# Kernel optimization log

Measured on AMD Instinct MI355X. Metric: run time of the kernel, lower is better.

## Reference

```python
import jax, jax.numpy as jnp
import numpy as np

N = 100000      # nodes
E = 3200000     # edges
F_IN = 128      # input node features
G = 64          # graphs in batch
A = 32          # action_shape


def _fanin_uniform(key, shape):
    v = 1.0 / np.sqrt(shape[0])
    return jax.random.uniform(key, shape, jnp.float32, -v, v)


def setup_inputs() -> dict:
    key = jax.random.key(0)
    ks = jax.random.split(key, 16)
    x = jax.random.normal(ks[0], (N, F_IN), jnp.float32)
    edge_index = jax.random.randint(ks[1], (2, E), 0, N, jnp.int64)
    batch = jnp.sort(jax.random.randint(ks[2], (N,), 0, G, jnp.int64))
    init_w = 0.003
    return {
        "x": x,
        "edge_index": edge_index,
        "batch": batch,
        # GCN weights are [in, out] (old-style PyG GCNConv .weight)
        "W1": _fanin_uniform(ks[3], (F_IN, 16)), "b1": jnp.zeros((16,), jnp.float32),
        "W2": _fanin_uniform(ks[4], (16, 64)),   "b2": jnp.zeros((64,), jnp.float32),
        "W3": _fanin_uniform(ks[5], (64, 32)),   "b3": jnp.zeros((32,), jnp.float32),
        # MLP head (Linear stores [out, in]; we keep [in, out] and matmul directly)
        "Wa": _fanin_uniform(ks[6], (32, 64)),   "ba": jnp.zeros((64,), jnp.float32),
        "Wo": jax.random.uniform(ks[7], (64, A), jnp.float32, -init_w, init_w),
        "bo": jnp.zeros((A,), jnp.float32),
    }


def _gcn_conv(x, W, b, src, dst, dinv):
    # GCNConv: D^{-1/2}(A+I)D^{-1/2} X W + b, symmetric norm with self-loops.
    h = x @ W                                   # [N, out] small GEMM
    coef = dinv[src] * dinv[dst]                # [E]
    msg = h[src] * coef[:, None]                # gather + scale (memory-bound)
    agg = jax.ops.segment_sum(msg, dst, num_segments=N)  # scatter-add
    agg = agg + h * (dinv * dinv)[:, None]      # self-loop contribution
    return agg + b


def reference(x, edge_index, batch, W1, b1, W2, b2, W3, b3, Wa, ba, Wo, bo):
    src, dst = edge_index[0], edge_index[1]
    # degree with self-loops (edge weights = 1)
    deg = jax.ops.segment_sum(jnp.ones((E,), x.dtype), dst, num_segments=N) + 1.0
    dinv = jax.lax.rsqrt(deg)

    h = jax.nn.relu(_gcn_conv(x, W1, b1, src, dst, dinv))   # dropout: eval no-op
    h = jax.nn.relu(_gcn_conv(h, W2, b2, src, dst, dinv))
    h = _gcn_conv(h, W3, b3, src, dst, dinv)                # [N, 32]

    # global_mean_pool over batch ids
    sums = jax.ops.segment_sum(h, batch, num_segments=G)            # [G, 32]
    cnts = jax.ops.segment_sum(jnp.ones((N,), h.dtype), batch, num_segments=G)
    pooled = sums / jnp.maximum(cnts, 1.0)[:, None]

    a = jax.nn.relu(pooled @ Wa + ba)
    return jnp.tanh(a @ Wo + bo)                             # [G, A]
```

## Files before the change

### kernel.cpp

```cpp
#include <hip/hip_runtime.h>
#include <hip/hip_bf16.h>
#include <math.h>


#define THREADS 256
#define TCSR 1024
#define BSH 8
#define MAXNB 512
#define CH_E 4096
#define CPT 8

typedef __attribute__((ext_vector_type(8))) short short8;
typedef __attribute__((ext_vector_type(4))) float f32x4;

__device__ inline unsigned short f2bf(float f) {
    unsigned int u = __float_as_uint(f);
    return (unsigned short)((u + 0x7fffu + ((u >> 16) & 1u)) >> 16);
}
__device__ inline unsigned int pk2bf(float a, float b) {
    return (unsigned int)f2bf(a) | ((unsigned int)f2bf(b) << 16);
}
__device__ inline float bflo(unsigned int u) { return __uint_as_float(u << 16); }
__device__ inline float bfhi(unsigned int u) { return __uint_as_float(u & 0xffff0000u); }
__device__ inline void unpk8(const uint4 u, float* f) {
    f[0] = bflo(u.x); f[1] = bfhi(u.x); f[2] = bflo(u.y); f[3] = bfhi(u.y);
    f[4] = bflo(u.z); f[5] = bfhi(u.z); f[6] = bflo(u.w); f[7] = bfhi(u.w);
}

__global__ void k_countA(const int* __restrict__ dst, unsigned short* __restrict__ lp16,
                         int* __restrict__ cnt_mat, int E, int NB, int NCH) {
    __shared__ int hist[MAXNB];
    int t = threadIdx.x, chunk = blockIdx.x;
    for (int h = t; h < NB; h += THREADS) hist[h] = 0;
    __syncthreads();
    int e0 = chunk * CH_E, e1 = min(E, e0 + CH_E);
    for (int e = e0 + t; e < e1; e += THREADS) {
        int h = dst[e] >> BSH;
        int lp = atomicAdd(&hist[h], 1);
        lp16[e] = (unsigned short)lp;
    }
    __syncthreads();
    for (int h = t; h < NB; h += THREADS) cnt_mat[(size_t)h * NCH + chunk] = hist[h];
}

__global__ void k_sumK1(const int* __restrict__ cnt_mat, int* __restrict__ bucket_tot, int NCH) {
    __shared__ int red[THREADS];
    int b = blockIdx.x, t = threadIdx.x;
    int s = 0;
    for (int c = t; c < NCH; c += THREADS) s += cnt_mat[(size_t)b * NCH + c];
    red[t] = s;
    __syncthreads();
    for (int off = THREADS / 2; off > 0; off >>= 1) {
        if (t < off) red[t] += red[t + off];
        __syncthreads();
    }
    if (t == 0) bucket_tot[b] = red[0];
}

__global__ void k_scanK2(const int* __restrict__ bucket_tot, int* __restrict__ bucket_base,
                         int* __restrict__ rowptr, float* __restrict__ sums,
                         int NB, int E, int N, int GS) {
    __shared__ int sh[MAXNB];
    int t = threadIdx.x;
    for (int i = t; i < GS; i += MAXNB) sums[i] = 0.0f;
    int v = (t < NB) ? bucket_tot[t] : 0;
    sh[t] = v;
    __syncthreads();
    for (int off = 1; off < MAXNB; off <<= 1) {
        int u = (t >= off) ? sh[t - off] : 0;
        __syncthreads();
        sh[t] += u;
        __syncthreads();
    }
    if (t < NB) bucket_base[t] = sh[t] - v;
    if (t == 0) { bucket_base[NB] = E; rowptr[N] = E; }
}

__global__ void k_scanK3(const int* __restrict__ cnt_mat, const int* __restrict__ bucket_base,
                         int* __restrict__ offs_mat, int NCH) {
    __shared__ int sh[THREADS];
    int b = blockIdx.x, t = threadIdx.x;
    int c0 = t * CPT;
    int v[CPT];
    int s = 0;
#pragma unroll
    for (int k = 0; k < CPT; ++k) {
        int c = c0 + k;
        v[k] = (c < NCH) ? cnt_mat[(size_t)b * NCH + c] : 0;
        s += v[k];
    }
    sh[t] = s;
    __syncthreads();
    for (int off = 1; off < THREADS; off <<= 1) {
        int u = (t >= off) ? sh[t - off] : 0;
        __syncthreads();
        sh[t] += u;
        __syncthreads();
    }
    int run = bucket_base[b] + sh[t] - s;
#pragma unroll
    for (int k = 0; k < CPT; ++k) {
        int c = c0 + k;
        if (c < NCH) { offs_mat[(size_t)b * NCH + c] = run; run += v[k]; }
    }
}

__global__ void k_scatter2(const int* __restrict__ src, const int* __restrict__ dst,
                           const unsigned short* __restrict__ lp16,
                           const int* __restrict__ offs_mat,
                           unsigned int* __restrict__ bedges, int E, int NB, int NCH) {
    __shared__ int offs[MAXNB];
    int t = threadIdx.x, chunk = blockIdx.x;
    for (int h = t; h < NB; h += THREADS) offs[h] = offs_mat[(size_t)h * NCH + chunk];
    __syncthreads();
    int e0 = chunk * CH_E, e1 = min(E, e0 + CH_E);
    for (int e = e0 + t; e < e1; e += THREADS) {
        int d = dst[e];
        int h = d >> BSH;
        int pos = offs[h] + (int)lp16[e];
        bedges[pos] = ((unsigned int)src[e] << BSH) | (unsigned int)(d & ((1 << BSH) - 1));
    }
}

__global__ __launch_bounds__(1024) void k_bucket_csr(const unsigned int* __restrict__ bedges,
                             const int* __restrict__ bucket_base,
                             int* __restrict__ rowptr, float* __restrict__ dinv,
                             int* __restrict__ csr_src, int N) {
    __shared__ int hist[256];
    __shared__ int sc[256];
    __shared__ int cur[256];
    int t = threadIdx.x;
    int b = blockIdx.x;
    int base = bucket_base[b];
    int end = bucket_base[b + 1];
    if (t < 256) hist[t] = 0;
    __syncthreads();
    for (int i = base + t; i < end; i += TCSR)
        atomicAdd(&hist[bedges[i] & 255], 1);
    __syncthreads();
    int c = 0;
    if (t < 256) { c = hist[t]; sc[t] = c; }
    __syncthreads();
    for (int off = 1; off < 256; off <<= 1) {
        int u = (t >= off && t < 256) ? sc[t - off] : 0;
        __syncthreads();
        if (t < 256) sc[t] += u;
        __syncthreads();
    }
    if (t < 256) {
        int excl = sc[t] - c;
        int node = (b << BSH) + t;
        if (node < N) {
            rowptr[node] = base + excl;
            dinv[node] = (float)(1.0 / sqrt((double)(c + 1)));
        }
        cur[t] = excl;
    }
    __syncthreads();
    for (int i = base + t; i < end; i += TCSR) {
        unsigned int u = bedges[i];
        int ln = (int)(u & 255);
        int p = atomicAdd(&cur[ln], 1);
        csr_src[base + p] = (int)(u >> BSH);
    }
}

__global__ __launch_bounds__(256) void k_gemm1(const float* __restrict__ X,
                        const float* __restrict__ W,
                        const float* __restrict__ dinv, unsigned short* __restrict__ H, int N) {
    __shared__ float Wt[16 * 128];
    int t = threadIdx.x;
    for (int i = t; i < 16 * 128; i += THREADS) {
        int j = i >> 7, k = i & 127;
        Wt[i] = W[k * 16 + j];
    }
    __syncthreads();
    int q = t & 3;
    int row = blockIdx.x * 64 + (t >> 2);
    if (row >= N) return;
    const float4* xr = (const float4*)(X + (size_t)row * 128);
    float acc[16];
#pragma unroll
    for (int j = 0; j < 16; ++j) acc[j] = 0.0f;
#pragma unroll
    for (int i = 0; i < 8; ++i) {
        int k4 = q + 4 * i;
        float4 xv = xr[k4];
#pragma unroll
        for (int j = 0; j < 16; ++j) {
            const float4 wv = *(const float4*)&Wt[j * 128 + k4 * 4];
            acc[j] += xv.x * wv.x + xv.y * wv.y + xv.z * wv.z + xv.w * wv.w;
        }
    }
#pragma unroll
    for (int j = 0; j < 16; ++j) {
        acc[j] += __shfl_xor(acc[j], 1);
        acc[j] += __shfl_xor(acc[j], 2);
    }
    if (q == 0) {
        float di = dinv[row];
        uint4 oa, ob;
        oa.x = pk2bf(acc[0] * di, acc[1] * di);
        oa.y = pk2bf(acc[2] * di, acc[3] * di);
        oa.z = pk2bf(acc[4] * di, acc[5] * di);
        oa.w = pk2bf(acc[6] * di, acc[7] * di);
        ob.x = pk2bf(acc[8] * di, acc[9] * di);
        ob.y = pk2bf(acc[10] * di, acc[11] * di);
        ob.z = pk2bf(acc[12] * di, acc[13] * di);
        ob.w = pk2bf(acc[14] * di, acc[15] * di);
        uint4* outr = (uint4*)(H + (size_t)row * 16);
        outr[0] = oa;
        outr[1] = ob;
    }
}

template<int F, int MODE, int S>
__global__ __launch_bounds__(256) void k_pull(
        const int* __restrict__ rowptr, const int* __restrict__ csr_src,
        const float* __restrict__ dinv, const unsigned short* __restrict__ Hb,
        const float* __restrict__ bias, void* __restrict__ outp,
        const int* __restrict__ batch, float* __restrict__ gsums,
        int N, int G) {
    const int LPN = F / 8;
    const int GRP = LPN * S;
    const int NPB = THREADS / GRP;
    int t = threadIdx.x;
    int idx = t % GRP;
    int fl = idx % LPN;
    int s  = idx / LPN;
    int fo = fl * 8;
    int node = blockIdx.x * NPB + t / GRP;

    float acc[8] = {0.f, 0.f, 0.f, 0.f, 0.f, 0.f, 0.f, 0.f};
    if (node < N) {
        int beg = rowptr[node], end = rowptr[node + 1];
        int i = beg + s;
        for (; i + 3 * S < end; i += 4 * S) {
            int s0 = csr_src[i];
            int s1 = csr_src[i + S];
            int s2 = csr_src[i + 2 * S];
            int s3 = csr_src[i + 3 * S];
            uint4 g0 = *(const uint4*)(Hb + (size_t)s0 * F + fo);
            uint4 g1 = *(const uint4*)(Hb + (size_t)s1 * F + fo);
            uint4 g2 = *(const uint4*)(Hb + (size_t)s2 * F + fo);
            uint4 g3 = *(const uint4*)(Hb + (size_t)s3 * F + fo);
            float f0[8], f1[8], f2[8], f3[8];
            unpk8(g0, f0); unpk8(g1, f1); unpk8(g2, f2); unpk8(g3, f3);
#pragma unroll
            for (int j = 0; j < 8; ++j) acc[j] += (f0[j] + f1[j]) + (f2[j] + f3[j]);
        }
        for (; i < end; i += S) {
            int sv = csr_src[i];
            uint4 g = *(const uint4*)(Hb + (size_t)sv * F + fo);
            float f[8];
            unpk8(g, f);
#pragma unroll
            for (int j = 0; j < 8; ++j) acc[j] += f[j];
        }
    }
#pragma unroll
    for (int j = 0; j < 8; ++j) {
        if (S >= 2) acc[j] += __shfl_xor(acc[j], LPN);
        if (S >= 4) acc[j] += __shfl_xor(acc[j], 2 * LPN);
    }

    if constexpr (MODE == 3) {
        __shared__ float lsum[4][32];
        __shared__ int g0s;
        for (int z = t; z < 4 * 32; z += THREADS) ((float*)lsum)[z] = 0.0f;
        if (t == 0) g0s = batch[blockIdx.x * NPB];
        __syncthreads();
        int g0 = g0s;
        if (node < N && s == 0) {
            uint4 gs = *(const uint4*)(Hb + (size_t)node * F + fo);
            float sf[8];
            unpk8(gs, sf);
            float di = dinv[node];
            int g = batch[node];
            int r = g - g0;
            if ((unsigned)r < 4u) {
#pragma unroll
                for (int j = 0; j < 8; ++j)
                    atomicAdd(&lsum[r][fo + j], di * (acc[j] + sf[j]));
            } else {
#pragma unroll
                for (int j = 0; j < 8; ++j)
                    atomicAdd(&gsums[(size_t)g * 32 + fo + j], di * (acc[j] + sf[j]));
            }
        }
        __syncthreads();
        if (t < 128) {
            int r = t >> 5, f = t & 31;
            int g = g0 + r;
            float v = lsum[r][f];
            if (g < G && v != 0.0f) atomicAdd(&gsums[(size_t)g * 32 + f], v);
        }
    } else {
        if (node < N && s == 0) {
            uint4 gs = *(const uint4*)(Hb + (size_t)node * F + fo);
            float sf[8];
            unpk8(gs, sf);
            float di = dinv[node];
            float tv[8];
#pragma unroll
            for (int j = 0; j < 8; ++j) tv[j] = di * (acc[j] + sf[j]);
            if constexpr (MODE == 1) {
                float w[8];
#pragma unroll
                for (int j = 0; j < 8; ++j) w[j] = fmaxf(tv[j] + bias[fo + j], 0.0f) * di;
                uint4 st;
                st.x = pk2bf(w[0], w[1]); st.y = pk2bf(w[2], w[3]);
                st.z = pk2bf(w[4], w[5]); st.w = pk2bf(w[6], w[7]);
                *(uint4*)((unsigned short*)outp + (size_t)node * F + fo) = st;
            } else {
                uint4 st;
                st.x = pk2bf(tv[0], tv[1]); st.y = pk2bf(tv[2], tv[3]);
                st.z = pk2bf(tv[4], tv[5]); st.w = pk2bf(tv[6], tv[7]);
                *(uint4*)((unsigned short*)outp + (size_t)node * F + fo) = st;
            }
        }
    }
}

__global__ __launch_bounds__(256) void k_mlp(const unsigned short* __restrict__ P2b,
                      const float* __restrict__ W2, const float* __restrict__ b2,
                      const float* __restrict__ W3, const float* __restrict__ dinv,
                      unsigned short* __restrict__ Hb3, int N) {
    __shared__ unsigned int aTd[4][32][17];
    int t = threadIdx.x;
    int w = t >> 6;
    int l = t & 63;
    int g = l >> 4;
    int c = l & 15;
    int node = blockIdx.x * 64 + w * 16 + c;
    bool nv = node < N;
    int cn = nv ? node : 0;

    short8 w2f[4];
#pragma unroll
    for (int mi = 0; mi < 4; ++mi) {
        short8 f = {0, 0, 0, 0, 0, 0, 0, 0};
        if (g < 2) {
            int j = 16 * mi + c;
#pragma unroll
            for (int e = 0; e < 8; ++e)
                f[e] = (short)f2bf(W2[(8 * g + e) * 64 + j]);
        }
        w2f[mi] = f;
    }
    short8 w3f[2][2];
#pragma unroll
    for (int mt = 0; mt < 2; ++mt)
#pragma unroll
        for (int kt = 0; kt < 2; ++kt) {
            short8 f;
#pragma unroll
            for (int e = 0; e < 8; ++e)
                f[e] = (short)f2bf(W3[(32 * kt + 8 * g + e) * 32 + 16 * mt + c]);
            w3f[mt][kt] = f;
        }
    float b2v[16];
#pragma unroll
    for (int mi = 0; mi < 4; ++mi)
#pragma unroll
        for (int r = 0; r < 4; ++r)
            b2v[4 * mi + r] = b2[16 * mi + 4 * g + r];

    short8 pf = {0, 0, 0, 0, 0, 0, 0, 0};
    if (g < 2) {
        pf = *(const short8*)(P2b + (size_t)cn * 16 + 8 * g);
    }

    f32x4 zero = {0.f, 0.f, 0.f, 0.f};
    f32x4 acc1[4];
#pragma unroll
    for (int mi = 0; mi < 4; ++mi)
        acc1[mi] = __builtin_amdgcn_mfma_f32_16x16x32_bf16(w2f[mi], pf, zero, 0, 0, 0);

#pragma unroll
    for (int mi = 0; mi < 4; ++mi) {
        float a0 = fmaxf(acc1[mi][0] + b2v[4 * mi + 0], 0.f);
        float a1 = fmaxf(acc1[mi][1] + b2v[4 * mi + 1], 0.f);
        float a2 = fmaxf(acc1[mi][2] + b2v[4 * mi + 2], 0.f);
        float a3 = fmaxf(acc1[mi][3] + b2v[4 * mi + 3], 0.f);
        aTd[w][8 * mi + 2 * g][c]     = pk2bf(a0, a1);
        aTd[w][8 * mi + 2 * g + 1][c] = pk2bf(a2, a3);
    }
    __syncthreads();

    short8 bfr[2];
#pragma unroll
    for (int kt = 0; kt < 2; ++kt) {
        short8 f;
#pragma unroll
        for (int i = 0; i < 4; ++i) {
            unsigned int d = aTd[w][16 * kt + 4 * g + i][c];
            f[2 * i]     = (short)(d & 0xffffu);
            f[2 * i + 1] = (short)(d >> 16);
        }
        bfr[kt] = f;
    }

    f32x4 acc2[2] = {{0.f, 0.f, 0.f, 0.f}, {0.f, 0.f, 0.f, 0.f}};
#pragma unroll
    for (int mt = 0; mt < 2; ++mt)
#pragma unroll
        for (int kt = 0; kt < 2; ++kt)
            acc2[mt] = __builtin_amdgcn_mfma_f32_16x16x32_bf16(w3f[mt][kt], bfr[kt], acc2[mt], 0, 0, 0);

    if (nv) {
        float di = dinv[node];
        unsigned short* o = Hb3 + (size_t)node * 32;
#pragma unroll
        for (int mt = 0; mt < 2; ++mt) {
            *(unsigned int*)(o + 16 * mt + 4 * g)     = pk2bf(acc2[mt][0] * di, acc2[mt][1] * di);
            *(unsigned int*)(o + 16 * mt + 4 * g + 2) = pk2bf(acc2[mt][2] * di, acc2[mt][3] * di);
        }
    }
}

__global__ void k_head(const float* __restrict__ sums, const int* __restrict__ batch, int N,
                       const float* __restrict__ b3,
                       const float* __restrict__ Wa, const float* __restrict__ ba,
                       const float* __restrict__ Wo, const float* __restrict__ bo,
                       float* __restrict__ out) {
    int g = blockIdx.x;
    int j = threadIdx.x;
    int lo = 0, hi = N;
    while (lo < hi) { int m = (lo + hi) >> 1; if (batch[m] < g) lo = m + 1; else hi = m; }
    int start = lo;
    lo = start; hi = N;
    while (lo < hi) { int m = (lo + hi) >> 1; if (batch[m] < g + 1) lo = m + 1; else hi = m; }
    int cnt = lo - start;
    float inv = 1.0f / (float)(cnt > 0 ? cnt : 1);

    __shared__ float p[32];
    __shared__ float a[64];
    if (j < 32) p[j] = sums[g * 32 + j] * inv + b3[j];
    __syncthreads();
    float acc = ba[j];
#pragma unroll
    for (int k = 0; k < 32; ++k) acc += p[k] * Wa[k * 64 + j];
    a[j] = fmaxf(acc, 0.0f);
    __syncthreads();
    if (j < 32) {
        float acc2 = bo[j];
#pragma unroll
        for (int k = 0; k < 64; ++k) acc2 += a[k] * Wo[k * 32 + j];
        out[g * 32 + j] = tanhf(acc2);
    }
}

static inline int cdiv(long long a, int b) { return (int)((a + b - 1) / b); }
static inline size_t align256(size_t x) { return (x + 255) & ~(size_t)255; }

extern "C" void kernel_launch(void* const* d_in, const int* in_sizes, int n_in,
                              void* d_out, int out_size, void* d_ws, size_t ws_size,
                              hipStream_t stream) {
    const float* x     = (const float*)d_in[0];
    const int*   edge  = (const int*)d_in[1];
    const int*   batch = (const int*)d_in[2];
    const float* W1 = (const float*)d_in[3];  const float* b1 = (const float*)d_in[4];
    const float* W2 = (const float*)d_in[5];  const float* b2 = (const float*)d_in[6];
    const float* W3 = (const float*)d_in[7];  const float* b3 = (const float*)d_in[8];
    const float* Wa = (const float*)d_in[9];  const float* ba = (const float*)d_in[10];
    const float* Wo = (const float*)d_in[11]; const float* bo = (const float*)d_in[12];

    const int E = in_sizes[1] / 2;
    const int N = in_sizes[2];
    const int G = 64;
    const int NB = cdiv(N, 1 << BSH);
    const int NCH = cdiv(E, CH_E);

    const int* srcp = edge;
    const int* dstp = edge + E;

    char* base = (char*)d_ws;
    size_t off = 0;
    float* dinv   = (float*)(base + off); off = align256(off + sizeof(float) * N);
    unsigned short* lp16 = (unsigned short*)(base + off); off = align256(off + sizeof(short) * E);
    int* cnt_mat  = (int*)(base + off); off = align256(off + sizeof(int) * (size_t)NB * NCH);
    int* offs_mat = (int*)(base + off); off = align256(off + sizeof(int) * (size_t)NB * NCH);
    int* btot     = (int*)(base + off); off = align256(off + sizeof(int) * (NB + 1));
    int* bbase    = (int*)(base + off); off = align256(off + sizeof(int) * (NB + 1));
    unsigned int* bedges = (unsigned int*)(base + off); off = align256(off + sizeof(int) * E);
    int* rowptr   = (int*)(base + off); off = align256(off + sizeof(int) * (N + 1));
    int* csr_src  = (int*)(base + off); off = align256(off + sizeof(int) * E);
    unsigned short* Hb1 = (unsigned short*)(base + off); off = align256(off + sizeof(short) * (size_t)N * 16);
    unsigned short* Hb2 = (unsigned short*)(base + off); off = align256(off + sizeof(short) * (size_t)N * 16);
    unsigned short* P2b = (unsigned short*)(base + off); off = align256(off + sizeof(short) * (size_t)N * 16);
    unsigned short* Hb3 = (unsigned short*)(base + off); off = align256(off + sizeof(short) * (size_t)N * 32);
    float* sums   = (float*)(base + off); off = align256(off + sizeof(float) * G * 32);

    k_countA<<<NCH, THREADS, 0, stream>>>(dstp, lp16, cnt_mat, E, NB, NCH);
    k_sumK1<<<NB, THREADS, 0, stream>>>(cnt_mat, btot, NCH);
    k_scanK2<<<1, MAXNB, 0, stream>>>(btot, bbase, rowptr, sums, NB, E, N, G * 32);
    k_scanK3<<<NB, THREADS, 0, stream>>>(cnt_mat, bbase, offs_mat, NCH);
    k_scatter2<<<NCH, THREADS, 0, stream>>>(srcp, dstp, lp16, offs_mat, bedges, E, NB, NCH);

    k_bucket_csr<<<NB, TCSR, 0, stream>>>(bedges, bbase, rowptr, dinv, csr_src, N);

    k_gemm1<<<cdiv(N, 64), THREADS, 0, stream>>>(x, W1, dinv, Hb1, N);
    k_pull<16, 1, 4><<<cdiv(N, 32), THREADS, 0, stream>>>(rowptr, csr_src, dinv, Hb1, b1, Hb2,
                                                          nullptr, nullptr, N, G);

    k_pull<16, 2, 4><<<cdiv(N, 32), THREADS, 0, stream>>>(rowptr, csr_src, dinv, Hb2, nullptr, P2b,
                                                          nullptr, nullptr, N, G);

    k_mlp<<<cdiv(N, 64), THREADS, 0, stream>>>(P2b, W2, b2, W3, dinv, Hb3, N);

    k_pull<32, 3, 2><<<cdiv(N, 32), THREADS, 0, stream>>>(rowptr, csr_src, dinv, Hb3, nullptr,
                                                          nullptr, batch, sums, N, G);

    k_head<<<G, 64, 0, stream>>>(sums, batch, N, b3, Wa, ba, Wo, bo, (float*)d_out);
}
```

Measured before the change: 307.5 us.

## Stage bucket scatter and CSR writes in LDS for coalesced global stores

The edge scatter kernel now computes per-chunk bucket offsets with an in-block scan and places the packed edges into shared memory in bucket order. It then writes them to global memory in runs that are contiguous within each bucket, instead of random scattered stores. The bucket CSR kernel likewise builds each bucket's sorted source list in LDS when it fits within a capacity, then copies it out contiguously. This adds more LDS (about 36KB and 35KB), an extra block scan and extra barriers, which may reduce occupancy.

```diff
diff --git a/kernel.cpp b/kernel.cpp
--- a/kernel.cpp
+++ b/kernel.cpp
@@ -9,6 +9,7 @@
 #define MAXNB 512
 #define CH_E 4096
 #define CPT 8
+#define CSR_CAP 8704
 
 typedef __attribute__((ext_vector_type(8))) short short8;
 typedef __attribute__((ext_vector_type(4))) float f32x4;
@@ -105,21 +106,47 @@
     }
 }
 
-__global__ void k_scatter2(const int* __restrict__ src, const int* __restrict__ dst,
-                           const unsigned short* __restrict__ lp16,
-                           const int* __restrict__ offs_mat,
-                           unsigned int* __restrict__ bedges, int E, int NB, int NCH) {
+__global__ __launch_bounds__(256) void k_scatter2(
+        const int* __restrict__ src, const int* __restrict__ dst,
+        const unsigned short* __restrict__ lp16,
+        const int* __restrict__ cnt_mat, const int* __restrict__ offs_mat,
+        unsigned int* __restrict__ bedges, int E, int NB, int NCH) {
     __shared__ int offs[MAXNB];
+    __shared__ int excl[MAXNB];
+    __shared__ unsigned int wbuf[CH_E];
+    __shared__ int gbuf[CH_E];
     int t = threadIdx.x, chunk = blockIdx.x;
-    for (int h = t; h < NB; h += THREADS) offs[h] = offs_mat[(size_t)h * NCH + chunk];
+    int c0 = (t < NB) ? cnt_mat[(size_t)t * NCH + chunk] : 0;
+    int c1 = (t + 256 < NB) ? cnt_mat[(size_t)(t + 256) * NCH + chunk] : 0;
+    if (t < NB) offs[t] = offs_mat[(size_t)t * NCH + chunk];
+    if (t + 256 < NB) offs[t + 256] = offs_mat[(size_t)(t + 256) * NCH + chunk];
+    excl[t] = c0;
+    excl[t + 256] = c1;
+    __syncthreads();
+    for (int off = 1; off < MAXNB; off <<= 1) {
+        int a = (t >= off) ? excl[t - off] : 0;
+        int b = (t + 256 >= off) ? excl[t + 256 - off] : 0;
+        __syncthreads();
+        excl[t] += a;
+        excl[t + 256] += b;
+        __syncthreads();
+    }
+    excl[t] -= c0;
+    excl[t + 256] -= c1;
     __syncthreads();
     int e0 = chunk * CH_E, e1 = min(E, e0 + CH_E);
+    int len = e1 - e0;
     for (int e = e0 + t; e < e1; e += THREADS) {
         int d = dst[e];
         int h = d >> BSH;
-        int pos = offs[h] + (int)lp16[e];
-        bedges[pos] = ((unsigned int)src[e] << BSH) | (unsigned int)(d & ((1 << BSH) - 1));
-    }
+        int lp = (int)lp16[e];
+        int s = excl[h] + lp;
+        wbuf[s] = ((unsigned int)src[e] << BSH) | (unsigned int)(d & ((1 << BSH) - 1));
+        gbuf[s] = offs[h] + lp;
+    }
+    __syncthreads();
+    for (int s = t; s < len; s += THREADS)
+        bedges[gbuf[s]] = wbuf[s];
 }
 
 __global__ __launch_bounds__(1024) void k_bucket_csr(const unsigned int* __restrict__ bedges,
@@ -129,10 +156,13 @@
     __shared__ int hist[256];
     __shared__ int sc[256];
     __shared__ int cur[256];
+    __shared__ int ssrc[CSR_CAP];
     int t = threadIdx.x;
     int b = blockIdx.x;
     int base = bucket_base[b];
     int end = bucket_base[b + 1];
+    int tot = end - base;
+    bool lds_ok = tot <= CSR_CAP;
     if (t < 256) hist[t] = 0;
     __syncthreads();
     for (int i = base + t; i < end; i += TCSR)
@@ -157,11 +187,23 @@
         cur[t] = excl;
     }
     __syncthreads();
-    for (int i = base + t; i < end; i += TCSR) {
-        unsigned int u = bedges[i];
-        int ln = (int)(u & 255);
-        int p = atomicAdd(&cur[ln], 1);
-        csr_src[base + p] = (int)(u >> BSH);
+    if (lds_ok) {
+        for (int i = base + t; i < end; i += TCSR) {
+            unsigned int u = bedges[i];
+            int ln = (int)(u & 255);
+            int p = atomicAdd(&cur[ln], 1);
+            ssrc[p] = (int)(u >> BSH);
+        }
+        __syncthreads();
+        for (int j = t; j < tot; j += TCSR)
+            csr_src[base + j] = ssrc[j];
+    } else {
+        for (int i = base + t; i < end; i += TCSR) {
+            unsigned int u = bedges[i];
+            int ln = (int)(u & 255);
+            int p = atomicAdd(&cur[ln], 1);
+            csr_src[base + p] = (int)(u >> BSH);
+        }
     }
 }
 
@@ -496,7 +538,7 @@
     k_sumK1<<<NB, THREADS, 0, stream>>>(cnt_mat, btot, NCH);
     k_scanK2<<<1, MAXNB, 0, stream>>>(btot, bbase, rowptr, sums, NB, E, N, G * 32);
     k_scanK3<<<NB, THREADS, 0, stream>>>(cnt_mat, bbase, offs_mat, NCH);
-    k_scatter2<<<NCH, THREADS, 0, stream>>>(srcp, dstp, lp16, offs_mat, bedges, E, NB, NCH);
+    k_scatter2<<<NCH, THREADS, 0, stream>>>(srcp, dstp, lp16, cnt_mat, offs_mat, bedges, E, NB, NCH);
 
     k_bucket_csr<<<NB, TCSR, 0, stream>>>(bedges, bbase, rowptr, dinv, csr_src, N);
 
```

New measurement: 283.6 us, median of 2. 1.08x faster.
